# Kernel tuning notes

Hardware: AMD Instinct MI355X
Metric: run time of the kernel (lower is better)

Reference implementation:

```python
import jax, jax.numpy as jnp
import numpy as np

FP8_MAX = 448.0   # e4m3 max (FP8Config.e4m3_max)
EPS = 1e-12       # FP8Config.eps
BLOCK = 128       # quantization block size


def block_quant_dequant(w, block_size=BLOCK, fp8_max=FP8_MAX):
    """DeepSeek-V3 style block-wise FP8 quantize->dequantize of weight [O, I].
    Scales are amax(block)/fp8_max; quant values clamped to [-fp8_max, fp8_max].
    Dims are exact multiples of block_size so no padding needed."""
    O, I = w.shape
    nb_o, nb_i = O // block_size, I // block_size
    # [nb_o, bs, nb_i, bs] -> [nb_o, nb_i, bs, bs]
    wb = w.reshape(nb_o, block_size, nb_i, block_size).transpose(0, 2, 1, 3)
    bmax = jnp.maximum(jnp.max(jnp.abs(wb), axis=(-2, -1), keepdims=True), EPS)
    scale = bmax / fp8_max  # per-block scale [nb_o, nb_i, 1, 1]
    q = jnp.clip(wb / scale, -fp8_max, fp8_max)  # fp8-representable values
    deq = q * scale
    return deq.transpose(0, 2, 1, 3).reshape(O, I)


def setup_inputs() -> dict:
    key = jax.random.key(0)
    k1, k2, k3 = jax.random.split(key, 3)
    B, S, D_IN, D_OUT = 4, 2048, 4096, 16384
    X = jax.random.normal(k1, (B, S, D_IN), dtype=jnp.float32)
    weight = jax.random.normal(k2, (D_OUT, D_IN), dtype=jnp.float32) * 0.02
    bias = jax.random.normal(k3, (D_OUT,), dtype=jnp.float32)
    return {"X": X, "weight": weight, "bias": bias}


def reference(X, weight, bias):
    # FP8Linear forward (non-triton path): W is block-quantized/dequantized,
    # then Y = X @ W_deq^T + b.
    W_deq = block_quant_dequant(weight)
    out = jnp.einsum('bsi,oi->bso', X, W_deq)
    return out + bias
```

## Files before the change

### kernel.cpp

```cpp
#include <hip/hip_runtime.h>
#include <stdint.h>
#include <stddef.h>


typedef _Float16 f16_t;
typedef _Float16 f16x8 __attribute__((ext_vector_type(8)));
typedef float    f32x4 __attribute__((ext_vector_type(4)));

#define BM 256
#define BN 256
#define BK 64

__global__ void __launch_bounds__(256) cvt_f32_to_f16(const float* __restrict__ src,
                                                      f16_t* __restrict__ dst,
                                                      int n8) {
    int i = blockIdx.x * 256 + threadIdx.x;
    if (i >= n8) return;
    const float4* s = (const float4*)src;
    float4 a = s[2 * i + 0];
    float4 b = s[2 * i + 1];
    f16x8 r;
    r[0] = (f16_t)a.x; r[1] = (f16_t)a.y; r[2] = (f16_t)a.z; r[3] = (f16_t)a.w;
    r[4] = (f16_t)b.x; r[5] = (f16_t)b.y; r[6] = (f16_t)b.z; r[7] = (f16_t)b.w;
    *(f16x8*)(dst + (size_t)i * 8) = r;
}

__device__ __forceinline__ void load_lds_16B(const f16_t* g, f16_t* l) {
    __builtin_amdgcn_global_load_lds(
        (const __attribute__((address_space(1))) void*)g,
        (__attribute__((address_space(3))) void*)l,
        16, 0, 0);
}

__global__ void __launch_bounds__(512, 2) gemm256_bias(const f16_t* __restrict__ A,
                                                       const f16_t* __restrict__ B,
                                                       const float* __restrict__ bias,
                                                       float* __restrict__ C,
                                                       int M, int N, int K) {
    __shared__ __align__(16) f16_t sA[2 * 2 * 128 * 64];
    __shared__ __align__(16) f16_t sB[2 * 2 * 128 * 64];

    const int tid  = threadIdx.x;
    const int w    = tid >> 6;
    const int l    = tid & 63;
    const int wr   = w >> 2;
    const int wc   = w & 3;
    const int l16  = l & 15;
    const int quad = l >> 4;
    const int bh   = wc >> 1;
    const int brow = (wc & 1) * 64;

    const int sw    = (l16 & 7) << 4;
    const int coff0 = (quad * 16) ^ sw;
    const int coff1 = (quad * 16 + 64) ^ sw;

    const int nwg = gridDim.x;
    const int q8  = nwg >> 3, r8 = nwg & 7;
    const int xcd = blockIdx.x & 7, off = blockIdx.x >> 3;
    const int swz = (xcd < r8 ? xcd * (q8 + 1) : r8 * (q8 + 1) + (xcd - r8) * q8) + off;
    const int MB  = M / BM;
    const int bm  = swz % MB;
    const int bn  = swz / MB;

    const int srow = w * 8 + (l >> 3);
    const int scol = 8 * ((l & 7) ^ ((l >> 3) & 7));
    const size_t stA = (size_t)(bm * BM + srow) * K + scol;
    const size_t stB = (size_t)(bn * BN + srow) * K + scol;
    f16_t* lwA = sA + w * 512;
    f16_t* lwB = sB + w * 512;

#define STAGE_A(d, h, tt) do {                                                  \
        const f16_t* g_ = A + stA + (size_t)((h) * 128) * K + (size_t)(tt) * 64; \
        f16_t* l_ = lwA + ((d) * 2 + (h)) * 8192;                               \
        load_lds_16B(g_, l_);                                                   \
        load_lds_16B(g_ + (size_t)64 * K, l_ + 4096);                           \
    } while (0)
#define STAGE_B(d, h, tt) do {                                                  \
        const f16_t* g_ = B + stB + (size_t)((h) * 128) * K + (size_t)(tt) * 64; \
        f16_t* l_ = lwB + ((d) * 2 + (h)) * 8192;                               \
        load_lds_16B(g_, l_);                                                   \
        load_lds_16B(g_ + (size_t)64 * K, l_ + 4096);                           \
    } while (0)

    const char* rdA = (const char*)sA + wr * 16384;
    const char* rdB = (const char*)sB + bh * 16384 + brow * 128;

    f16x8 as[4][2];
    f16x8 b0[2][2], b1[2][2];
    f32x4 acc[8][4];
#pragma unroll
    for (int i = 0; i < 8; ++i)
#pragma unroll
        for (int j = 0; j < 4; ++j)
            acc[i][j] = (f32x4){0.f, 0.f, 0.f, 0.f};

#define LD_A(d, mibase) do { _Pragma("unroll")                                  \
        for (int i_ = 0; i_ < 4; ++i_) {                                        \
            const char* p_ = rdA + (d) * 32768 + (((mibase) + i_) * 16 + l16) * 128; \
            as[i_][0] = *(const f16x8*)(p_ + coff0);                            \
            as[i_][1] = *(const f16x8*)(p_ + coff1);                            \
        } } while (0)
#define LD_B(d, nibase, dst) do { _Pragma("unroll")                             \
        for (int n_ = 0; n_ < 2; ++n_) {                                        \
            const char* p_ = rdB + (d) * 32768 + (((nibase) + n_) * 16 + l16) * 128; \
            dst[n_][0] = *(const f16x8*)(p_ + coff0);                           \
            dst[n_][1] = *(const f16x8*)(p_ + coff1);                           \
        } } while (0)

#define MF(mibase, nibase, bset) do { _Pragma("unroll")                         \
        for (int i_ = 0; i_ < 4; ++i_) { _Pragma("unroll")                      \
            for (int n_ = 0; n_ < 2; ++n_) { _Pragma("unroll")                  \
                for (int k_ = 0; k_ < 2; ++k_)                                  \
                    acc[(mibase) + i_][(nibase) + n_] =                         \
                        __builtin_amdgcn_mfma_f32_16x16x32_f16(                 \
                            as[i_][k_], bset[n_][k_],                           \
                            acc[(mibase) + i_][(nibase) + n_], 0, 0, 0);        \
            } } } while (0)

#define WAIT_LGKM() do { asm volatile("s_waitcnt lgkmcnt(0)" ::: "memory");     \
        __builtin_amdgcn_sched_barrier(0); } while (0)
#define BAR() __builtin_amdgcn_s_barrier()

    const int KT  = K / BK;
    const int NIT = KT / 2;

    STAGE_B(0, 0, 0); STAGE_B(0, 1, 0);
    STAGE_A(0, 0, 0); STAGE_A(0, 1, 0);
    STAGE_B(1, 0, 1); STAGE_B(1, 1, 1);

    for (int it = 0; it < NIT; ++it) {
        const int t01 = 2 * it + 1;
        int t23 = 2 * it + 2; if (t23 > KT - 1) t23 = KT - 1;
        int t67 = 2 * it + 3; if (t67 > KT - 1) t67 = KT - 1;

        STAGE_A(1, 0, t01);
        asm volatile("s_waitcnt vmcnt(6)" ::: "memory");
        BAR();
        LD_A(0, 0); LD_B(0, 0, b0);
        WAIT_LGKM();
        __builtin_amdgcn_s_setprio(1);
        MF(0, 0, b0);
        __builtin_amdgcn_s_setprio(0);
        BAR();
        LD_B(0, 2, b1);
        STAGE_A(1, 1, t01);
        BAR();
        WAIT_LGKM();
        __builtin_amdgcn_s_setprio(1);
        MF(0, 2, b1);
        __builtin_amdgcn_s_setprio(0);
        BAR();
        LD_A(0, 4);
        STAGE_B(0, 0, t23);
        BAR();
        WAIT_LGKM();
        __builtin_amdgcn_s_setprio(1);
        MF(4, 0, b0);
        __builtin_amdgcn_s_setprio(0);
        BAR();
        STAGE_B(0, 1, t23);
        BAR();
        __builtin_amdgcn_s_setprio(1);
        MF(4, 2, b1);
        __builtin_amdgcn_s_setprio(0);
        BAR();
        STAGE_A(0, 0, t23);
        asm volatile("s_waitcnt vmcnt(6)" ::: "memory");
        BAR();
        LD_A(1, 0); LD_B(1, 0, b0);
        WAIT_LGKM();
        __builtin_amdgcn_s_setprio(1);
        MF(0, 0, b0);
        __builtin_amdgcn_s_setprio(0);
        BAR();
        LD_B(1, 2, b1);
        STAGE_A(0, 1, t23);
        BAR();
        WAIT_LGKM();
        __builtin_amdgcn_s_setprio(1);
        MF(0, 2, b1);
        __builtin_amdgcn_s_setprio(0);
        BAR();
        LD_A(1, 4);
        STAGE_B(1, 0, t67);
        BAR();
        WAIT_LGKM();
        __builtin_amdgcn_s_setprio(1);
        MF(4, 0, b0);
        __builtin_amdgcn_s_setprio(0);
        BAR();
        STAGE_B(1, 1, t67);
        BAR();
        __builtin_amdgcn_s_setprio(1);
        MF(4, 2, b1);
        __builtin_amdgcn_s_setprio(0);
        BAR();
    }

    asm volatile("s_waitcnt vmcnt(0)" ::: "memory");

    const int c0 = bn * BN + wc * 64;
    const int r0 = bm * BM + wr * 128;
#pragma unroll
    for (int ni = 0; ni < 4; ++ni) {
        const int col = c0 + ni * 16 + l16;
        const float bv = bias[col];
#pragma unroll
        for (int mi = 0; mi < 8; ++mi) {
            const int row0 = r0 + mi * 16 + quad * 4;
            float* cp = C + (size_t)row0 * N + col;
#pragma unroll
            for (int r = 0; r < 4; ++r)
                cp[(size_t)r * N] = acc[mi][ni][r] + bv;
        }
    }
}

extern "C" void kernel_launch(void* const* d_in, const int* in_sizes, int n_in,
                              void* d_out, int out_size, void* d_ws, size_t ws_size,
                              hipStream_t stream) {
    const float* X    = (const float*)d_in[0];
    const float* W    = (const float*)d_in[1];
    const float* bias = (const float*)d_in[2];
    float* out        = (float*)d_out;

    const int N = in_sizes[2];
    const int K = in_sizes[1] / N;
    const int M = in_sizes[0] / K;

    f16_t* Xh = (f16_t*)d_ws;
    f16_t* Wh = Xh + (size_t)M * K;

    const int nx8 = (M * K) / 8;
    const int nw8 = (N * K) / 8;
    cvt_f32_to_f16<<<dim3((nx8 + 255) / 256), 256, 0, stream>>>(X, Xh, nx8);
    cvt_f32_to_f16<<<dim3((nw8 + 255) / 256), 256, 0, stream>>>(W, Wh, nw8);

    const int nblk = (M / BM) * (N / BN);
    gemm256_bias<<<dim3(nblk), dim3(512), 0, stream>>>(Xh, Wh, bias, out, M, N, K);
}
```

Before: 2.106 ms.

## Restructure GEMM main loop staging schedule and vmcnt waits

```diff
diff --git a/kernel.cpp b/kernel.cpp
--- a/kernel.cpp
+++ b/kernel.cpp
@@ -120,6 +120,8 @@
 #define WAIT_LGKM() do { asm volatile("s_waitcnt lgkmcnt(0)" ::: "memory");     \
         __builtin_amdgcn_sched_barrier(0); } while (0)
 #define BAR() __builtin_amdgcn_s_barrier()
+#define PRIO_MF(mi, ni, bs) do { __builtin_amdgcn_s_setprio(1);                 \
+        MF(mi, ni, bs); __builtin_amdgcn_s_setprio(0); } while (0)
 
     const int KT  = K / BK;
     const int NIT = KT / 2;
@@ -127,73 +129,55 @@
     STAGE_B(0, 0, 0); STAGE_B(0, 1, 0);
     STAGE_A(0, 0, 0); STAGE_A(0, 1, 0);
     STAGE_B(1, 0, 1); STAGE_B(1, 1, 1);
+    asm volatile("s_waitcnt vmcnt(4)" ::: "memory");
+    BAR();
 
     for (int it = 0; it < NIT; ++it) {
-        const int t01 = 2 * it + 1;
-        int t23 = 2 * it + 2; if (t23 > KT - 1) t23 = KT - 1;
-        int t67 = 2 * it + 3; if (t67 > KT - 1) t67 = KT - 1;
-
-        STAGE_A(1, 0, t01);
-        asm volatile("s_waitcnt vmcnt(6)" ::: "memory");
-        BAR();
+        const int tU = 2 * it + 1;
+        int tV = 2 * it + 2; if (tV > KT - 1) tV = KT - 1;
+        int tW = 2 * it + 3; if (tW > KT - 1) tW = KT - 1;
+
         LD_A(0, 0); LD_B(0, 0, b0);
-        WAIT_LGKM();
-        __builtin_amdgcn_s_setprio(1);
-        MF(0, 0, b0);
-        __builtin_amdgcn_s_setprio(0);
+        STAGE_A(1, 0, tU); STAGE_A(1, 1, tU);
+        BAR();
+        WAIT_LGKM();
+        PRIO_MF(0, 0, b0);
         BAR();
         LD_B(0, 2, b1);
-        STAGE_A(1, 1, t01);
-        BAR();
-        WAIT_LGKM();
-        __builtin_amdgcn_s_setprio(1);
-        MF(0, 2, b1);
-        __builtin_amdgcn_s_setprio(0);
+        BAR();
+        WAIT_LGKM();
+        PRIO_MF(0, 2, b1);
         BAR();
         LD_A(0, 4);
-        STAGE_B(0, 0, t23);
-        BAR();
-        WAIT_LGKM();
-        __builtin_amdgcn_s_setprio(1);
-        MF(4, 0, b0);
-        __builtin_amdgcn_s_setprio(0);
-        BAR();
-        STAGE_B(0, 1, t23);
-        BAR();
-        __builtin_amdgcn_s_setprio(1);
-        MF(4, 2, b1);
-        __builtin_amdgcn_s_setprio(0);
-        BAR();
-        STAGE_A(0, 0, t23);
-        asm volatile("s_waitcnt vmcnt(6)" ::: "memory");
+        STAGE_B(0, 0, tV); STAGE_B(0, 1, tV);
+        BAR();
+        WAIT_LGKM();
+        PRIO_MF(4, 0, b0);
+        BAR();
+        asm volatile("s_waitcnt vmcnt(4)" ::: "memory");
+        BAR();
+        PRIO_MF(4, 2, b1);
         BAR();
         LD_A(1, 0); LD_B(1, 0, b0);
-        WAIT_LGKM();
-        __builtin_amdgcn_s_setprio(1);
-        MF(0, 0, b0);
-        __builtin_amdgcn_s_setprio(0);
+        STAGE_A(0, 0, tV); STAGE_A(0, 1, tV);
+        BAR();
+        WAIT_LGKM();
+        PRIO_MF(0, 0, b0);
         BAR();
         LD_B(1, 2, b1);
-        STAGE_A(0, 1, t23);
-        BAR();
-        WAIT_LGKM();
-        __builtin_amdgcn_s_setprio(1);
-        MF(0, 2, b1);
-        __builtin_amdgcn_s_setprio(0);
+        BAR();
+        WAIT_LGKM();
+        PRIO_MF(0, 2, b1);
         BAR();
         LD_A(1, 4);
-        STAGE_B(1, 0, t67);
-        BAR();
-        WAIT_LGKM();
-        __builtin_amdgcn_s_setprio(1);
-        MF(4, 0, b0);
-        __builtin_amdgcn_s_setprio(0);
-        BAR();
-        STAGE_B(1, 1, t67);
-        BAR();
-        __builtin_amdgcn_s_setprio(1);
-        MF(4, 2, b1);
-        __builtin_amdgcn_s_setprio(0);
+        STAGE_B(1, 0, tW); STAGE_B(1, 1, tW);
+        BAR();
+        WAIT_LGKM();
+        PRIO_MF(4, 0, b0);
+        BAR();
+        asm volatile("s_waitcnt vmcnt(4)" ::: "memory");
+        BAR();
+        PRIO_MF(4, 2, b1);
         BAR();
     }
 
```

Result: faster. 1.947 ms (-7.6%).
